# Performance work log

Measured on AMD Instinct MI355X. Metric: run time of the kernel, lower is better.

Reference implementation:

```python
import jax, jax.numpy as jnp
import numpy as np

B, HC, WC, KC = 4, 32, 32, 1024   # coarse feature map (ResNet101 layer3)
HF, WF, KF = 128, 128, 256        # fine feature map (ResNet101 layer1)
DC = 4                            # downscale_coef; HF // DC == HC


def setup_inputs() -> dict:
    key = jax.random.key(0)
    k1, k2, k3, k4 = jax.random.split(key, 4)
    return {
        "F_g1_coarse": jax.random.normal(k1, (B, HC, WC, KC), jnp.float32),
        "F_gk_coarse": jax.random.normal(k2, (B, HC, WC, KC), jnp.float32),
        "F_g1_fine": jax.random.normal(k3, (B, HF, WF, KF), jnp.float32),
        "F_gk_fine": jax.random.normal(k4, (B, HF, WF, KF), jnp.float32),
    }


def _coarse_match(f1, fk):
    # For every coarse position in Gk find nearest (L2) coarse position in G1.
    b, h, w, k = f1.shape
    a = f1.reshape(b, h * w, k)   # G1 positions
    q = fk.reshape(b, h * w, k)   # Gk positions
    # ||q||^2 + ||a||^2 - 2 q.a  -> [B, HW_gk, HW_g1]
    d = ((q * q).sum(-1)[:, :, None]
         + (a * a).sum(-1)[:, None, :]
         - 2.0 * jnp.einsum('bnk,bmk->bnm', q, a))
    idx = jnp.argmin(d, axis=-1)                       # [B, HW]
    cm = jnp.stack([idx // w, idx % w], axis=-1)       # (row, col) in G1
    return cm.reshape(b, h, w, 2).astype(jnp.int32)


def _fine_match(f1, fk, cm, dc):
    # Refine each dc x dc fine tile of Gk by searching the fine pixels of G1
    # covered by the coarse matches of the 3x3 coarse-neighborhood.
    b, h, w, k = fk.shape
    hc, wc = h // dc, w // dc
    off = jnp.arange(-1, 2)
    nI = jnp.clip(jnp.arange(hc)[:, None] + off[None, :], 0, hc - 1)  # [Hc,3]
    nJ = jnp.clip(jnp.arange(wc)[:, None] + off[None, :], 0, wc - 1)  # [Wc,3]
    # neighbor coarse matches: [B, Hc, Wc, 3, 3, 2]
    nb = cm[:, nI[:, None, :, None], nJ[None, :, None, :]]
    nb = nb.reshape(b, hc, wc, 9, 2)
    # expand each coarse match to its dc*dc fine pixels in G1
    sr = jnp.repeat(jnp.arange(dc), dc)   # [dc^2] row shifts
    sc = jnp.tile(jnp.arange(dc), dc)     # [dc^2] col shifts
    ncand = 9 * dc * dc                   # 144 candidates per tile
    cand_r = (nb[..., 0][..., None] * dc + sr).reshape(b, hc, wc, ncand)
    cand_c = (nb[..., 1][..., None] * dc + sc).reshape(b, hc, wc, ncand)
    # gather candidate fine features from G1: [B, Hc, Wc, N, K]
    bi = jnp.arange(b)[:, None, None, None]
    cand_f = f1[bi, cand_r, cand_c]
    # fine tile features of Gk: [B, Hc, Wc, dc^2, K]
    fkb = fk.reshape(b, hc, dc, wc, dc, k).transpose(0, 1, 3, 2, 4, 5)
    fkb = fkb.reshape(b, hc, wc, dc * dc, k)
    dist = ((fkb * fkb).sum(-1)[..., :, None]
            + (cand_f * cand_f).sum(-1)[..., None, :]
            - 2.0 * jnp.einsum('bhwpk,bhwnk->bhwpn', fkb, cand_f))
    best = jnp.argmin(dist, axis=-1)      # [B, Hc, Wc, dc^2]
    hi = jnp.arange(hc)[None, :, None, None]
    wi = jnp.arange(wc)[None, None, :, None]
    best_r = cand_r[bi, hi, wi, best]     # [B, Hc, Wc, dc^2]
    best_c = cand_c[bi, hi, wi, best]
    def to_grid(x):
        return x.reshape(b, hc, wc, dc, dc).transpose(0, 1, 3, 2, 4).reshape(b, h, w)
    return jnp.stack([to_grid(best_r), to_grid(best_c)], axis=-1).astype(jnp.int32)


def reference(F_g1_coarse, F_gk_coarse, F_g1_fine, F_gk_fine):
    closest_coarse = _coarse_match(F_g1_coarse, F_gk_coarse)   # [B,Hc,Wc,2]
    closest_fine = _fine_match(F_g1_fine, F_gk_fine, closest_coarse, DC)  # [B,H,W,2]
    return closest_coarse, closest_fine
```

## Files before the change

### kernel.cpp

```cpp
#include <hip/hip_runtime.h>
#include <cstdint>
#include <cstddef>

#define BB 4
#define HCC 32
#define WCC 32
#define KCC 1024
#define NCC (HCC*WCC)
#define HFF 128
#define WFF 128
#define KFF 256
#define DCC 4
#define NCHUNK 8

typedef _Float16 half8 __attribute__((ext_vector_type(8)));
typedef _Float16 half4_t __attribute__((ext_vector_type(4)));
typedef float f32x4 __attribute__((ext_vector_type(4)));
#define MFMA16(a,b,c) __builtin_amdgcn_mfma_f32_16x16x32_f16((a),(b),(c),0,0,0)
#define INV2K 0.00048828125f

__device__ inline void cvt8(const float4 u0, const float4 u1, half8& h, half8& l2) {
  float uu[8];
  *(float4*)uu = u0; *(float4*)(uu + 4) = u1;
  #pragma unroll
  for (int e = 0; e < 8; ++e) {
    _Float16 hh = (_Float16)uu[e];
    float r = (uu[e] - (float)hh) * 2048.0f;
    h[e] = hh; l2[e] = (_Float16)r;
  }
}

template<int K>
__global__ __launch_bounds__(256) void preconv_kernel(
    const float* __restrict__ src0, const float* __restrict__ src1,
    _Float16* __restrict__ hi0, _Float16* __restrict__ lo0,
    _Float16* __restrict__ hi1, _Float16* __restrict__ lo1,
    float* __restrict__ nr0, float* __restrict__ nr1, int rows) {
  const float* __restrict__ src = blockIdx.y ? src1 : src0;
  _Float16* __restrict__ hi = blockIdx.y ? hi1 : hi0;
  _Float16* __restrict__ lo = blockIdx.y ? lo1 : lo0;
  float* __restrict__ nrm = blockIdx.y ? nr1 : nr0;
  const int wave = threadIdx.x >> 6, lane = threadIdx.x & 63;
  const int row = blockIdx.x * 4 + wave;
  if (row >= rows) return;
  const float* p = src + (size_t)row * K;
  const size_t ob = (size_t)row * K + lane * 4;
  float s = 0.f;
  #pragma unroll
  for (int c = 0; c < K / 256; ++c) {
    float4 v = *(const float4*)(p + c * 256 + lane * 4);
    s += v.x*v.x + v.y*v.y + v.z*v.z + v.w*v.w;
    float vv[4] = {v.x, v.y, v.z, v.w};
    half4_t h, l2;
    #pragma unroll
    for (int e = 0; e < 4; ++e) {
      _Float16 hh = (_Float16)vv[e];
      l2[e] = (_Float16)((vv[e] - (float)hh) * 2048.0f);
      h[e] = hh;
    }
    *(half4_t*)(hi + ob + c * 256) = h;
    *(half4_t*)(lo + ob + c * 256) = l2;
  }
  #pragma unroll
  for (int m = 1; m <= 32; m <<= 1) s += __shfl_xor(s, m, 64);
  if (lane == 0) nrm[row] = s;
}

__global__ __launch_bounds__(256) void preconv_fine_kernel(
    const float* __restrict__ src, _Float16* __restrict__ hl,
    float* __restrict__ nrm, int rows) {
  const int wave = threadIdx.x >> 6, lane = threadIdx.x & 63;
  const int row = blockIdx.x * 4 + wave;
  if (row >= rows) return;
  float4 v = *(const float4*)(src + (size_t)row * KFF + lane * 4);
  float s = v.x*v.x + v.y*v.y + v.z*v.z + v.w*v.w;
  float vv[4] = {v.x, v.y, v.z, v.w};
  half4_t h, l2;
  #pragma unroll
  for (int e = 0; e < 4; ++e) {
    _Float16 hh = (_Float16)vv[e];
    l2[e] = (_Float16)((vv[e] - (float)hh) * 2048.0f);
    h[e] = hh;
  }
  const size_t dst = (size_t)row * 512 + (lane >> 3) * 64 + ((lane >> 1) & 3) * 16 + (lane & 1) * 4;
  *(half4_t*)(hl + dst)     = h;
  *(half4_t*)(hl + dst + 8) = l2;
  #pragma unroll
  for (int m = 1; m <= 32; m <<= 1) s += __shfl_xor(s, m, 64);
  if (lane == 0) nrm[row] = s;
}

__global__ __launch_bounds__(256, 2) void coarse_kernel2(
    const _Float16* __restrict__ gAhi, const _Float16* __restrict__ gAlo,
    const _Float16* __restrict__ gBhi, const _Float16* __restrict__ gBlo,
    const float* __restrict__ na, const float* __restrict__ nq,
    float* __restrict__ pval, int* __restrict__ pidx) {
  __shared__ _Float16 Ahi[128][64], Alo[128][64];
  __shared__ _Float16 Bhi[64][64],  Blo[64][64];
  __shared__ float a2s[128], q2s[64];
  __shared__ float redv[2][64];
  __shared__ int   redi[2][64];

  const int t = threadIdx.x;
  const int chunk = blockIdx.x;
  const int n0 = blockIdx.y * 64;
  const int b  = blockIdx.z;
  const int m0 = chunk * 128;

  const int ar = t >> 1, ahf = t & 1;
  const int brw = t >> 2, bq = t & 3;
  const int l  = t & 63;
  const int wv = t >> 6;
  const int wm = wv >> 1, wn = wv & 1;

  if (t < 128) a2s[t] = na[b*NCC + m0 + t];
  else if (t < 192) q2s[t - 128] = nq[b*NCC + n0 + (t - 128)];

  const _Float16* __restrict__ gah = gAhi + (size_t)(b*NCC + m0 + ar) * KCC + ahf * 32;
  const _Float16* __restrict__ gal = gAlo + (size_t)(b*NCC + m0 + ar) * KCC + ahf * 32;
  const _Float16* __restrict__ gbh = gBhi + (size_t)(b*NCC + n0 + brw) * KCC + bq * 16;
  const _Float16* __restrict__ gbl = gBlo + (size_t)(b*NCC + n0 + brw) * KCC + bq * 16;

  f32x4 accA[4][2], accB[4][2];
  #pragma unroll
  for (int mt = 0; mt < 4; ++mt)
    #pragma unroll
    for (int nt = 0; nt < 2; ++nt) { accA[mt][nt] = (f32x4)0.f; accB[mt][nt] = (f32x4)0.f; }

  for (int k0 = 0; k0 < KCC; k0 += 64) {
    __syncthreads();
    #pragma unroll
    for (int c2 = 0; c2 < 4; ++c2) {
      half8 h  = *(const half8*)(gah + k0 + c2 * 8);
      half8 l8 = *(const half8*)(gal + k0 + c2 * 8);
      int cs = (ahf * 4 + c2) ^ (ar & 7);
      *(half8*)&Ahi[ar][cs * 8] = h;
      *(half8*)&Alo[ar][cs * 8] = l8;
    }
    #pragma unroll
    for (int c2 = 0; c2 < 2; ++c2) {
      half8 h  = *(const half8*)(gbh + k0 + c2 * 8);
      half8 l8 = *(const half8*)(gbl + k0 + c2 * 8);
      int cs = (bq * 2 + c2) ^ (brw & 7);
      *(half8*)&Bhi[brw][cs * 8] = h;
      *(half8*)&Blo[brw][cs * 8] = l8;
    }
    __syncthreads();

    #pragma unroll
    for (int kk = 0; kk < 2; ++kk) {
      const int cs = ((kk * 4 + (l >> 4)) ^ (l & 7)) * 8;
      half8 ah[4], al[4], bh[2], bl[2];
      #pragma unroll
      for (int mt = 0; mt < 4; ++mt) {
        int row = wm * 64 + mt * 16 + (l & 15);
        ah[mt] = *(const half8*)&Ahi[row][cs];
        al[mt] = *(const half8*)&Alo[row][cs];
      }
      #pragma unroll
      for (int nt = 0; nt < 2; ++nt) {
        int row = wn * 32 + nt * 16 + (l & 15);
        bh[nt] = *(const half8*)&Bhi[row][cs];
        bl[nt] = *(const half8*)&Blo[row][cs];
      }
      #pragma unroll
      for (int mt = 0; mt < 4; ++mt)
        #pragma unroll
        for (int nt = 0; nt < 2; ++nt) {
          accA[mt][nt] = MFMA16(ah[mt], bh[nt], accA[mt][nt]);
          accB[mt][nt] = MFMA16(ah[mt], bl[nt], accB[mt][nt]);
          accB[mt][nt] = MFMA16(al[mt], bh[nt], accB[mt][nt]);
        }
    }
  }

  #pragma unroll
  for (int nt = 0; nt < 2; ++nt) {
    float q2 = q2s[wn * 32 + nt * 16 + (l & 15)];
    float bv = 3.0e38f; int bi = 0;
    #pragma unroll
    for (int mt = 0; mt < 4; ++mt)
      #pragma unroll
      for (int r = 0; r < 4; ++r) {
        float dot = accA[mt][nt][r] + accB[mt][nt][r] * INV2K;
        int ml = wm * 64 + mt * 16 + (l >> 4) * 4 + r;
        float d = (q2 + a2s[ml]) - 2.0f * dot;
        if (d < bv) { bv = d; bi = m0 + ml; }
      }
    #pragma unroll
    for (int mm = 16; mm < 64; mm <<= 1) {
      float ov = __shfl_xor(bv, mm, 64);
      int oi = __shfl_xor(bi, mm, 64);
      if (ov < bv || (ov == bv && oi < bi)) { bv = ov; bi = oi; }
    }
    if ((l >> 4) == 0) { redv[wm][wn*32 + nt*16 + l] = bv; redi[wm][wn*32 + nt*16 + l] = bi; }
  }
  __syncthreads();
  if (t < 64) {
    float v0 = redv[0][t]; int i0 = redi[0][t];
    float v1 = redv[1][t]; int i1 = redi[1][t];
    if (v1 < v0) { v0 = v1; i0 = i1; }
    pval[((size_t)b * NCC + n0 + t) * NCHUNK + chunk] = v0;
    pidx[((size_t)b * NCC + n0 + t) * NCHUNK + chunk] = i0;
  }
}

__global__ __launch_bounds__(256) void coarse_reduce_kernel(
    const float* __restrict__ pval, const int* __restrict__ pidx,
    int* __restrict__ out) {
  int g = blockIdx.x * 256 + threadIdx.x;
  if (g >= BB * NCC) return;
  float bv = pval[(size_t)g * NCHUNK];
  int bi = pidx[(size_t)g * NCHUNK];
  #pragma unroll
  for (int c = 1; c < NCHUNK; ++c) {
    float v = pval[(size_t)g * NCHUNK + c];
    int ix = pidx[(size_t)g * NCHUNK + c];
    if (v < bv) { bv = v; bi = ix; }
  }
  out[(size_t)g*2]     = bi >> 5;
  out[(size_t)g*2 + 1] = bi & 31;
}

__global__ __launch_bounds__(1024, 4) void fine_kernel4(
    const _Float16* __restrict__ gHL, const float* __restrict__ fkf,
    const float* __restrict__ naf, const int* __restrict__ coarse,
    int* __restrict__ outf) {
  __shared__ _Float16 CS[576 * 64];
  __shared__ _Float16 QS[256 * 64];
  __shared__ int   rIdx[576];
  __shared__ float tNORM[576];
  __shared__ float QN4[256][4];
  __shared__ int cbr[36], cbc[36];

  const int t = threadIdx.x;
  const int bx = blockIdx.x, by = blockIdx.y, b = blockIdx.z;
  const int l = t & 63, w = t >> 6;
  const int cy = w >> 2, cx = w & 3;
  const int ii = by * 4 + cy, jj = bx * 4 + cx;

  if (t < 36) {
    int wy = t / 6, wx = t % 6;
    int y = min(max(by * 4 - 1 + wy, 0), HCC - 1);
    int x = min(max(bx * 4 - 1 + wx, 0), WCC - 1);
    int base = ((b * HCC + y) * WCC + x) * 2;
    cbr[t] = coarse[base]; cbc[t] = coarse[base + 1];
  }
  __syncthreads();
  if (t < 576) {
    int slot = t >> 4, s = t & 15;
    int row = cbr[slot] * DCC + (s >> 2), col = cbc[slot] * DCC + (s & 3);
    int g = (b * HFF + row) * WFF + col;
    rIdx[t] = g; tNORM[t] = naf[g];
  }
  const int qrow = t >> 2, qpart = t & 3;
  const int qcell = qrow >> 4, qs = qrow & 15;
  const int qfr = (by * 4 + (qcell >> 2)) * DCC + (qs >> 2);
  const int qfc = (bx * 4 + (qcell & 3)) * DCC + (qs & 3);
  const float* qsrc = fkf + ((size_t)(b * HFF + qfr) * WFF + qfc) * KFF + qpart * 8;
  const int qswz = qrow & 7;
  float qnp = 0.f;
  __syncthreads();

  f32x4 accA[9], accB[9];
  #pragma unroll
  for (int T = 0; T < 9; ++T) { accA[T] = (f32x4)0.f; accB[T] = (f32x4)0.f; }

  const int q = l >> 4, r = l & 15;
  const int rsw = r & 7;
  const int woff[9] = {0, 1, 2, 6, 7, 8, 12, 13, 14};
  const int wbase = cy * 6 + cx;

  for (int ke = 0; ke < 8; ++ke) {
    #pragma unroll
    for (int it = 0; it < 5; ++it) {
      int g2 = it * 1024 + t;
      if (g2 < 4608) {
        int rowG = g2 >> 3, lc = g2 & 7;
        const _Float16* src = gHL + (size_t)rIdx[rowG] * 512 + ke * 64
                              + (lc >> 1) * 16 + (lc & 1) * 8;
        half8 v = *(const half8*)src;
        *(half8*)&CS[rowG * 64 + (lc ^ (rowG & 7)) * 8] = v;
      }
    }
    {
      float4 u0 = *(const float4*)(qsrc + ke * 32);
      float4 u1 = *(const float4*)(qsrc + ke * 32 + 4);
      qnp += u0.x*u0.x + u0.y*u0.y + u0.z*u0.z + u0.w*u0.w
           + u1.x*u1.x + u1.y*u1.y + u1.z*u1.z + u1.w*u1.w;
      half8 hh, hl;
      cvt8(u0, u1, hh, hl);
      *(half8*)&QS[qrow * 64 + ((qpart * 2)     ^ qswz) * 8] = hh;
      *(half8*)&QS[qrow * 64 + ((qpart * 2 + 1) ^ qswz) * 8] = hl;
      if (ke == 7) { QN4[qrow][qpart] = qnp; }
    }
    __syncthreads();
    half8 bh = *(const half8*)&QS[(w * 16 + r) * 64 + ((q * 2)     ^ rsw) * 8];
    half8 bl = *(const half8*)&QS[(w * 16 + r) * 64 + ((q * 2 + 1) ^ rsw) * 8];
    #pragma unroll
    for (int T = 0; T < 9; ++T) {
      int rowG = (wbase + woff[T]) * 16 + r;
      half8 ah = *(const half8*)&CS[rowG * 64 + ((q * 2)     ^ rsw) * 8];
      half8 al = *(const half8*)&CS[rowG * 64 + ((q * 2 + 1) ^ rsw) * 8];
      accA[T] = MFMA16(ah, bh, accA[T]);
      accB[T] = MFMA16(ah, bl, accB[T]);
      accB[T] = MFMA16(al, bh, accB[T]);
    }
    __syncthreads();
  }

  {
    float q2v = QN4[w * 16 + r][0] + QN4[w * 16 + r][1]
              + QN4[w * 16 + r][2] + QN4[w * 16 + r][3];
    float bv = 3.0e38f; int bi = 0;
    #pragma unroll
    for (int T = 0; T < 9; ++T) {
      int slot = wbase + woff[T];
      #pragma unroll
      for (int r2 = 0; r2 < 4; ++r2) {
        int s4 = q * 4 + r2;
        float cn = tNORM[slot * 16 + s4];
        float dot = accA[T][r2] + accB[T][r2] * INV2K;
        float d = (q2v + cn) - 2.0f * dot;
        int m = T * 16 + s4;
        if (d < bv) { bv = d; bi = m; }
      }
    }
    #pragma unroll
    for (int mm = 16; mm < 64; mm <<= 1) {
      float ov = __shfl_xor(bv, mm, 64);
      int oi = __shfl_xor(bi, mm, 64);
      if (ov < bv || (ov == bv && oi < bi)) { bv = ov; bi = oi; }
    }
    if (l < 16) {
      int T = bi >> 4, s3 = bi & 15, slot = wbase + woff[T];
      int br = cbr[slot] * DCC + (s3 >> 2);
      int bc = cbc[slot] * DCC + (s3 & 3);
      int fr = ii * DCC + (l >> 2), fc = jj * DCC + (l & 3);
      size_t ob = ((size_t)(b * HFF + fr) * WFF + fc) * 2;
      outf[ob]     = br;
      outf[ob + 1] = bc;
    }
  }
}

__global__ __launch_bounds__(256, 2) void coarse_kernel(
    const float* __restrict__ f1, const float* __restrict__ fk,
    float* __restrict__ pval, int* __restrict__ pidx) {
  __shared__ _Float16 Ahi[128][64], Alo[128][64];
  __shared__ _Float16 Bhi[64][64],  Blo[64][64];
  __shared__ float npA[256], npB[256];
  __shared__ float a2s[128], q2s[64];
  __shared__ float redv[2][64];
  __shared__ int   redi[2][64];

  const int t = threadIdx.x;
  const int chunk = blockIdx.x;
  const int n0 = blockIdx.y * 64;
  const int b  = blockIdx.z;
  const int m0 = chunk * 128;

  const float* __restrict__ Abase = f1 + ((size_t)b * NCC + m0) * KCC;
  const float* __restrict__ Bbase = fk + ((size_t)b * NCC + n0) * KCC;

  const int ar = t >> 1, ahf = t & 1;
  const int brw = t >> 2, bq = t & 3;
  const int l  = t & 63;
  const int wv = t >> 6;
  const int wm = wv >> 1, wn = wv & 1;

  float nrmA = 0.f, nrmB = 0.f;
  f32x4 accA[4][2], accB[4][2];
  #pragma unroll
  for (int mt = 0; mt < 4; ++mt)
    #pragma unroll
    for (int nt = 0; nt < 2; ++nt) { accA[mt][nt] = (f32x4)0.f; accB[mt][nt] = (f32x4)0.f; }

  for (int k0 = 0; k0 < KCC; k0 += 64) {
    __syncthreads();
    {
      const float4* src = (const float4*)(Abase + (size_t)ar * KCC + k0 + ahf * 32);
      float4 va[8];
      #pragma unroll
      for (int i2 = 0; i2 < 8; ++i2) va[i2] = src[i2];
      #pragma unroll
      for (int i2 = 0; i2 < 8; ++i2)
        nrmA += va[i2].x*va[i2].x + va[i2].y*va[i2].y + va[i2].z*va[i2].z + va[i2].w*va[i2].w;
      #pragma unroll
      for (int c2 = 0; c2 < 4; ++c2) {
        half8 hh, hl;
        cvt8(va[c2*2], va[c2*2+1], hh, hl);
        int cs = (ahf * 4 + c2) ^ (ar & 7);
        *(half8*)&Ahi[ar][cs * 8] = hh;
        *(half8*)&Alo[ar][cs * 8] = hl;
      }
    }
    {
      const float4* src = (const float4*)(Bbase + (size_t)brw * KCC + k0 + bq * 16);
      float4 vb[4];
      #pragma unroll
      for (int i2 = 0; i2 < 4; ++i2) vb[i2] = src[i2];
      #pragma unroll
      for (int i2 = 0; i2 < 4; ++i2)
        nrmB += vb[i2].x*vb[i2].x + vb[i2].y*vb[i2].y + vb[i2].z*vb[i2].z + vb[i2].w*vb[i2].w;
      #pragma unroll
      for (int c2 = 0; c2 < 2; ++c2) {
        half8 hh, hl;
        cvt8(vb[c2*2], vb[c2*2+1], hh, hl);
        int cs = (bq * 2 + c2) ^ (brw & 7);
        *(half8*)&Bhi[brw][cs * 8] = hh;
        *(half8*)&Blo[brw][cs * 8] = hl;
      }
    }
    __syncthreads();

    #pragma unroll
    for (int kk = 0; kk < 2; ++kk) {
      const int cs = ((kk * 4 + (l >> 4)) ^ (l & 7)) * 8;
      half8 ah[4], al[4], bh[2], bl[2];
      #pragma unroll
      for (int mt = 0; mt < 4; ++mt) {
        int row = wm * 64 + mt * 16 + (l & 15);
        ah[mt] = *(const half8*)&Ahi[row][cs];
        al[mt] = *(const half8*)&Alo[row][cs];
      }
      #pragma unroll
      for (int nt = 0; nt < 2; ++nt) {
        int row = wn * 32 + nt * 16 + (l & 15);
        bh[nt] = *(const half8*)&Bhi[row][cs];
        bl[nt] = *(const half8*)&Blo[row][cs];
      }
      #pragma unroll
      for (int mt = 0; mt < 4; ++mt)
        #pragma unroll
        for (int nt = 0; nt < 2; ++nt) {
          accA[mt][nt] = MFMA16(ah[mt], bh[nt], accA[mt][nt]);
          accB[mt][nt] = MFMA16(ah[mt], bl[nt], accB[mt][nt]);
          accB[mt][nt] = MFMA16(al[mt], bh[nt], accB[mt][nt]);
        }
    }
  }

  npA[t] = nrmA; npB[t] = nrmB;
  __syncthreads();
  if (t < 128) a2s[t] = npA[2*t] + npA[2*t + 1];
  if (t < 64)  q2s[t] = npB[4*t] + npB[4*t + 1] + npB[4*t + 2] + npB[4*t + 3];
  __syncthreads();

  #pragma unroll
  for (int nt = 0; nt < 2; ++nt) {
    float q2 = q2s[wn * 32 + nt * 16 + (l & 15)];
    float bv = 3.0e38f; int bi = 0;
    #pragma unroll
    for (int mt = 0; mt < 4; ++mt)
      #pragma unroll
      for (int r = 0; r < 4; ++r) {
        float dot = accA[mt][nt][r] + accB[mt][nt][r] * INV2K;
        int ml = wm * 64 + mt * 16 + (l >> 4) * 4 + r;
        float d = (q2 + a2s[ml]) - 2.0f * dot;
        if (d < bv) { bv = d; bi = m0 + ml; }
      }
    #pragma unroll
    for (int mm = 16; mm < 64; mm <<= 1) {
      float ov = __shfl_xor(bv, mm, 64);
      int oi = __shfl_xor(bi, mm, 64);
      if (ov < bv || (ov == bv && oi < bi)) { bv = ov; bi = oi; }
    }
    if ((l >> 4) == 0) { redv[wm][wn*32 + nt*16 + l] = bv; redi[wm][wn*32 + nt*16 + l] = bi; }
  }
  __syncthreads();
  if (t < 64) {
    float v0 = redv[0][t]; int i0 = redi[0][t];
    float v1 = redv[1][t]; int i1 = redi[1][t];
    if (v1 < v0) { v0 = v1; i0 = i1; }
    pval[((size_t)b * NCC + n0 + t) * NCHUNK + chunk] = v0;
    pidx[((size_t)b * NCC + n0 + t) * NCHUNK + chunk] = i0;
  }
}

__global__ __launch_bounds__(192) void fine_kernel(
    const float* __restrict__ f1, const float* __restrict__ fkf,
    const int* __restrict__ coarse, int* __restrict__ outf) {
  __shared__ _Float16 Qhi[16][256], Qlo[16][256];
  __shared__ float qn[16], cn[144];
  __shared__ int cROW[144];
  __shared__ int cbr[9], cbc[9];
  __shared__ float redv[3][16];
  __shared__ int   redi[3][16];

  const int t = threadIdx.x;
  const int j = blockIdx.x, i = blockIdx.y, b = blockIdx.z;
  const int l = t & 63, wv = t >> 6;

  if (t < 9) {
    int di = t / 3 - 1, dj = t % 3 - 1;
    int y = min(max(i + di, 0), HCC - 1);
    int x = min(max(j + dj, 0), WCC - 1);
    int base = ((b*HCC + y)*WCC + x) * 2;
    cbr[t] = coarse[base];
    cbc[t] = coarse[base + 1];
  }
  __syncthreads();
  if (t < 144) {
    int n9 = t >> 4, s = t & 15;
    int row = cbr[n9]*DCC + (s >> 2), col = cbc[n9]*DCC + (s & 3);
    cROW[t] = (b*HFF + row)*WFF + col;
  }
  if (t < 64) {
    int qr = l & 15, qq = l >> 4;
    int fr = i*DCC + (qr >> 2), fc = j*DCC + (qr & 3);
    const float* src = fkf + ((size_t)(b*HFF + fr)*WFF + fc) * KFF + qq * 64;
    float s2 = 0.f;
    #pragma unroll
    for (int c2 = 0; c2 < 8; ++c2) {
      float4 u0 = *(const float4*)(src + c2*8);
      float4 u1 = *(const float4*)(src + c2*8 + 4);
      s2 += u0.x*u0.x + u0.y*u0.y + u0.z*u0.z + u0.w*u0.w
          + u1.x*u1.x + u1.y*u1.y + u1.z*u1.z + u1.w*u1.w;
      half8 hh, hl;
      cvt8(u0, u1, hh, hl);
      int cs = (qq * 8 + c2) ^ (qr & 7);
      *(half8*)&Qhi[qr][cs * 8] = hh;
      *(half8*)&Qlo[qr][cs * 8] = hl;
    }
    s2 += __shfl_xor(s2, 16, 64);
    s2 += __shfl_xor(s2, 32, 64);
    if (qq == 0) qn[qr] = s2;
  }
  __syncthreads();

  const float* ap[3];
  #pragma unroll
  for (int T = 0; T < 3; ++T)
    ap[T] = f1 + (size_t)cROW[(wv*3 + T)*16 + (l & 15)] * KFF;

  f32x4 accA[3], accB[3];
  float nrmp[3];
  #pragma unroll
  for (int T = 0; T < 3; ++T) { accA[T] = (f32x4)0.f; accB[T] = (f32x4)0.f; nrmp[T] = 0.f; }

  #pragma unroll 2
  for (int s = 0; s < 8; ++s) {
    const int cs = ((s * 4 + (l >> 4)) ^ (l & 7)) * 8;
    half8 bh = *(const half8*)&Qhi[l & 15][cs];
    half8 bl = *(const half8*)&Qlo[l & 15][cs];
    #pragma unroll
    for (int T = 0; T < 3; ++T) {
      const float* p = ap[T] + s*32 + (l >> 4)*8;
      float4 u0 = *(const float4*)p;
      float4 u1 = *(const float4*)(p + 4);
      nrmp[T] += u0.x*u0.x + u0.y*u0.y + u0.z*u0.z + u0.w*u0.w
               + u1.x*u1.x + u1.y*u1.y + u1.z*u1.z + u1.w*u1.w;
      half8 ahv, alv;
      cvt8(u0, u1, ahv, alv);
      accA[T] = MFMA16(ahv, bh, accA[T]);
      accB[T] = MFMA16(ahv, bl, accB[T]);
      accB[T] = MFMA16(alv, bh, accB[T]);
    }
  }

  #pragma unroll
  for (int T = 0; T < 3; ++T) {
    float np = nrmp[T];
    np += __shfl_xor(np, 16, 64);
    np += __shfl_xor(np, 32, 64);
    if ((l >> 4) == 0) cn[(wv*3 + T)*16 + l] = np;
  }
  __syncthreads();

  {
    float q2 = qn[l & 15];
    float bv = 3.0e38f; int bi = 0;
    #pragma unroll
    for (int T = 0; T < 3; ++T)
      #pragma unroll
      for (int r = 0; r < 4; ++r) {
        float dot = accA[T][r] + accB[T][r] * INV2K;
        int m = (wv*3 + T)*16 + (l >> 4)*4 + r;
        float d = (q2 + cn[m]) - 2.0f * dot;
        if (d < bv) { bv = d; bi = m; }
      }
    #pragma unroll
    for (int mm = 16; mm < 64; mm <<= 1) {
      float ov = __shfl_xor(bv, mm, 64);
      int oi = __shfl_xor(bi, mm, 64);
      if (ov < bv || (ov == bv && oi < bi)) { bv = ov; bi = oi; }
    }
    if ((l >> 4) == 0 && l < 16) { redv[wv][l] = bv; redi[wv][l] = bi; }
  }
  __syncthreads();

  if (t < 16) {
    float v = redv[0][t]; int ix = redi[0][t];
    #pragma unroll
    for (int w = 1; w < 3; ++w) {
      float ov = redv[w][t];
      if (ov < v) { v = ov; ix = redi[w][t]; }
    }
    int n9 = ix >> 4, s3 = ix & 15;
    int br = cbr[n9]*DCC + (s3 >> 2);
    int bc = cbc[n9]*DCC + (s3 & 3);
    int fr = i*DCC + (t >> 2), fc = j*DCC + (t & 3);
    size_t ob = ((size_t)(b*HFF + fr)*WFF + fc) * 2;
    outf[ob]     = br;
    outf[ob + 1] = bc;
  }
}

extern "C" void kernel_launch(void* const* d_in, const int* in_sizes, int n_in,
                              void* d_out, int out_size, void* d_ws, size_t ws_size,
                              hipStream_t stream) {
  (void)in_sizes; (void)n_in; (void)out_size;
  const float* f1c = (const float*)d_in[0];
  const float* fkc = (const float*)d_in[1];
  const float* f1f = (const float*)d_in[2];
  const float* fkf = (const float*)d_in[3];
  int* out = (int*)d_out;

  const size_t NEED = 101220352;
  if (ws_size >= NEED) {
    char* w = (char*)d_ws;
    _Float16* cAhi = (_Float16*)(w);
    _Float16* cAlo = (_Float16*)(w + 8388608);
    _Float16* cBhi = (_Float16*)(w + 16777216);
    _Float16* cBlo = (_Float16*)(w + 25165824);
    _Float16* fHL  = (_Float16*)(w + 33554432);
    float* na_c = (float*)(w + 100663296);
    float* nq_c = (float*)(w + 100679680);
    float* na_f = (float*)(w + 100696064);
    float* pval = (float*)(w + 100958208);
    int*   pidx = (int*)  (w + 101089280);

    preconv_kernel<KCC><<<dim3(BB*NCC/4, 2), 256, 0, stream>>>(
        f1c, fkc, cAhi, cAlo, cBhi, cBlo, na_c, nq_c, BB*NCC);
    preconv_fine_kernel<<<dim3(BB*HFF*WFF/4), 256, 0, stream>>>(
        f1f, fHL, na_f, BB*HFF*WFF);
    coarse_kernel2<<<dim3(NCHUNK, NCC/64, BB), 256, 0, stream>>>(
        cAhi, cAlo, cBhi, cBlo, na_c, nq_c, pval, pidx);
    coarse_reduce_kernel<<<dim3((BB*NCC + 255)/256), 256, 0, stream>>>(pval, pidx, out);
    fine_kernel4<<<dim3(WCC/4, HCC/4, BB), 1024, 0, stream>>>(
        fHL, fkf, na_f, out, out + BB*NCC*2);
  } else {
    float* pval = (float*)d_ws;
    int*   pidx = (int*)((float*)d_ws + BB*NCC*NCHUNK);
    coarse_kernel<<<dim3(NCHUNK, NCC/64, BB), 256, 0, stream>>>(f1c, fkc, pval, pidx);
    coarse_reduce_kernel<<<dim3((BB*NCC + 255)/256), 256, 0, stream>>>(pval, pidx, out);
    fine_kernel<<<dim3(WCC, HCC, BB), 192, 0, stream>>>(f1f, fkf, out, out + BB*NCC*2);
  }
}
```

Measured before the change: 118.2 us.

## Register-prefetch next K tiles in coarse and fine kernels, shrink fine blocks

Both the coarse GEMM kernel and the fine matching kernel now load the next K-slice from global memory into registers while MFMAs run on the current shared-memory tile, hiding global load latency. The fine kernel is also reshaped from 1024-thread blocks covering 4x4 coarse cells to 512-thread blocks covering 2x4 cells. It precomputes gather offsets and drops the trailing barrier. This costs more registers and reloads more halo candidates per output, and the relaxed launch bounds may lower occupancy.

```diff
diff --git a/kernel.cpp b/kernel.cpp
--- a/kernel.cpp
+++ b/kernel.cpp
@@ -90,7 +90,7 @@
   if (lane == 0) nrm[row] = s;
 }
 
-__global__ __launch_bounds__(256, 2) void coarse_kernel2(
+__global__ __launch_bounds__(256) void coarse_kernel3(
     const _Float16* __restrict__ gAhi, const _Float16* __restrict__ gAlo,
     const _Float16* __restrict__ gBhi, const _Float16* __restrict__ gBlo,
     const float* __restrict__ na, const float* __restrict__ nq,
@@ -127,25 +127,40 @@
     #pragma unroll
     for (int nt = 0; nt < 2; ++nt) { accA[mt][nt] = (f32x4)0.f; accB[mt][nt] = (f32x4)0.f; }
 
+  half8 pah[4], pal[4], pbh[2], pbl[2];
+  #pragma unroll
+  for (int c2 = 0; c2 < 4; ++c2) { pah[c2] = *(const half8*)(gah + c2*8); pal[c2] = *(const half8*)(gal + c2*8); }
+  #pragma unroll
+  for (int c2 = 0; c2 < 2; ++c2) { pbh[c2] = *(const half8*)(gbh + c2*8); pbl[c2] = *(const half8*)(gbl + c2*8); }
+
   for (int k0 = 0; k0 < KCC; k0 += 64) {
     __syncthreads();
     #pragma unroll
     for (int c2 = 0; c2 < 4; ++c2) {
-      half8 h  = *(const half8*)(gah + k0 + c2 * 8);
-      half8 l8 = *(const half8*)(gal + k0 + c2 * 8);
       int cs = (ahf * 4 + c2) ^ (ar & 7);
-      *(half8*)&Ahi[ar][cs * 8] = h;
-      *(half8*)&Alo[ar][cs * 8] = l8;
+      *(half8*)&Ahi[ar][cs * 8] = pah[c2];
+      *(half8*)&Alo[ar][cs * 8] = pal[c2];
     }
     #pragma unroll
     for (int c2 = 0; c2 < 2; ++c2) {
-      half8 h  = *(const half8*)(gbh + k0 + c2 * 8);
-      half8 l8 = *(const half8*)(gbl + k0 + c2 * 8);
       int cs = (bq * 2 + c2) ^ (brw & 7);
-      *(half8*)&Bhi[brw][cs * 8] = h;
-      *(half8*)&Blo[brw][cs * 8] = l8;
+      *(half8*)&Bhi[brw][cs * 8] = pbh[c2];
+      *(half8*)&Blo[brw][cs * 8] = pbl[c2];
     }
     __syncthreads();
+
+    if (k0 + 64 < KCC) {
+      #pragma unroll
+      for (int c2 = 0; c2 < 4; ++c2) {
+        pah[c2] = *(const half8*)(gah + k0 + 64 + c2*8);
+        pal[c2] = *(const half8*)(gal + k0 + 64 + c2*8);
+      }
+      #pragma unroll
+      for (int c2 = 0; c2 < 2; ++c2) {
+        pbh[c2] = *(const half8*)(gbh + k0 + 64 + c2*8);
+        pbl[c2] = *(const half8*)(gbl + k0 + 64 + c2*8);
+      }
+    }
 
     #pragma unroll
     for (int kk = 0; kk < 2; ++kk) {
@@ -222,45 +237,60 @@
   out[(size_t)g*2 + 1] = bi & 31;
 }
 
-__global__ __launch_bounds__(1024, 4) void fine_kernel4(
+__global__ __launch_bounds__(512) void fine_kernel5(
     const _Float16* __restrict__ gHL, const float* __restrict__ fkf,
     const float* __restrict__ naf, const int* __restrict__ coarse,
     int* __restrict__ outf) {
-  __shared__ _Float16 CS[576 * 64];
-  __shared__ _Float16 QS[256 * 64];
-  __shared__ int   rIdx[576];
-  __shared__ float tNORM[576];
-  __shared__ float QN4[256][4];
-  __shared__ int cbr[36], cbc[36];
+  __shared__ _Float16 CS[384 * 64];
+  __shared__ _Float16 QS[128 * 64];
+  __shared__ int   rIdx[384];
+  __shared__ float tNORM[384];
+  __shared__ float QN4[128][4];
+  __shared__ int cbr[24], cbc[24];
 
   const int t = threadIdx.x;
   const int bx = blockIdx.x, by = blockIdx.y, b = blockIdx.z;
   const int l = t & 63, w = t >> 6;
   const int cy = w >> 2, cx = w & 3;
-  const int ii = by * 4 + cy, jj = bx * 4 + cx;
-
-  if (t < 36) {
+  const int ii = by * 2 + cy, jj = bx * 4 + cx;
+
+  if (t < 24) {
     int wy = t / 6, wx = t % 6;
-    int y = min(max(by * 4 - 1 + wy, 0), HCC - 1);
+    int y = min(max(by * 2 - 1 + wy, 0), HCC - 1);
     int x = min(max(bx * 4 - 1 + wx, 0), WCC - 1);
     int base = ((b * HCC + y) * WCC + x) * 2;
     cbr[t] = coarse[base]; cbc[t] = coarse[base + 1];
   }
   __syncthreads();
-  if (t < 576) {
+  if (t < 384) {
     int slot = t >> 4, s = t & 15;
     int row = cbr[slot] * DCC + (s >> 2), col = cbc[slot] * DCC + (s & 3);
     int g = (b * HFF + row) * WFF + col;
     rIdx[t] = g; tNORM[t] = naf[g];
   }
+  __syncthreads();
+
+  unsigned srcOff[6], dstOff[6];
+  #pragma unroll
+  for (int it = 0; it < 6; ++it) {
+    int g2 = it * 512 + t;
+    int rowG = g2 >> 3, lc = g2 & 7;
+    srcOff[it] = (unsigned)rIdx[rowG] * 512u + (unsigned)((lc >> 1) * 16 + (lc & 1) * 8);
+    dstOff[it] = (unsigned)(rowG * 64 + (lc ^ (rowG & 7)) * 8);
+  }
   const int qrow = t >> 2, qpart = t & 3;
   const int qcell = qrow >> 4, qs = qrow & 15;
-  const int qfr = (by * 4 + (qcell >> 2)) * DCC + (qs >> 2);
+  const int qfr = (by * 2 + (qcell >> 2)) * DCC + (qs >> 2);
   const int qfc = (bx * 4 + (qcell & 3)) * DCC + (qs & 3);
   const float* qsrc = fkf + ((size_t)(b * HFF + qfr) * WFF + qfc) * KFF + qpart * 8;
   const int qswz = qrow & 7;
   float qnp = 0.f;
-  __syncthreads();
+
+  half8 pf[6];
+  #pragma unroll
+  for (int it = 0; it < 6; ++it) pf[it] = *(const half8*)(gHL + srcOff[it]);
+  float4 qu0 = *(const float4*)(qsrc);
+  float4 qu1 = *(const float4*)(qsrc + 4);
 
   f32x4 accA[9], accB[9];
   #pragma unroll
@@ -272,29 +302,28 @@
   const int wbase = cy * 6 + cx;
 
   for (int ke = 0; ke < 8; ++ke) {
-    #pragma unroll
-    for (int it = 0; it < 5; ++it) {
-      int g2 = it * 1024 + t;
-      if (g2 < 4608) {
-        int rowG = g2 >> 3, lc = g2 & 7;
-        const _Float16* src = gHL + (size_t)rIdx[rowG] * 512 + ke * 64
-                              + (lc >> 1) * 16 + (lc & 1) * 8;
-        half8 v = *(const half8*)src;
-        *(half8*)&CS[rowG * 64 + (lc ^ (rowG & 7)) * 8] = v;
-      }
-    }
+    __syncthreads();
+    #pragma unroll
+    for (int it = 0; it < 6; ++it) *(half8*)&CS[dstOff[it]] = pf[it];
     {
-      float4 u0 = *(const float4*)(qsrc + ke * 32);
-      float4 u1 = *(const float4*)(qsrc + ke * 32 + 4);
-      qnp += u0.x*u0.x + u0.y*u0.y + u0.z*u0.z + u0.w*u0.w
-           + u1.x*u1.x + u1.y*u1.y + u1.z*u1.z + u1.w*u1.w;
+      qnp += qu0.x*qu0.x + qu0.y*qu0.y + qu0.z*qu0.z + qu0.w*qu0.w
+           + qu1.x*qu1.x + qu1.y*qu1.y + qu1.z*qu1.z + qu1.w*qu1.w;
       half8 hh, hl;
-      cvt8(u0, u1, hh, hl);
+      cvt8(qu0, qu1, hh, hl);
       *(half8*)&QS[qrow * 64 + ((qpart * 2)     ^ qswz) * 8] = hh;
       *(half8*)&QS[qrow * 64 + ((qpart * 2 + 1) ^ qswz) * 8] = hl;
-      if (ke == 7) { QN4[qrow][qpart] = qnp; }
+      if (ke == 7) QN4[qrow][qpart] = qnp;
     }
     __syncthreads();
+
+    if (ke < 7) {
+      #pragma unroll
+      for (int it = 0; it < 6; ++it)
+        pf[it] = *(const half8*)(gHL + srcOff[it] + (unsigned)(ke + 1) * 64u);
+      qu0 = *(const float4*)(qsrc + (ke + 1) * 32);
+      qu1 = *(const float4*)(qsrc + (ke + 1) * 32 + 4);
+    }
+
     half8 bh = *(const half8*)&QS[(w * 16 + r) * 64 + ((q * 2)     ^ rsw) * 8];
     half8 bl = *(const half8*)&QS[(w * 16 + r) * 64 + ((q * 2 + 1) ^ rsw) * 8];
     #pragma unroll
@@ -306,7 +335,6 @@
       accB[T] = MFMA16(ah, bl, accB[T]);
       accB[T] = MFMA16(al, bh, accB[T]);
     }
-    __syncthreads();
   }
 
   {
@@ -635,10 +663,10 @@
         f1c, fkc, cAhi, cAlo, cBhi, cBlo, na_c, nq_c, BB*NCC);
     preconv_fine_kernel<<<dim3(BB*HFF*WFF/4), 256, 0, stream>>>(
         f1f, fHL, na_f, BB*HFF*WFF);
-    coarse_kernel2<<<dim3(NCHUNK, NCC/64, BB), 256, 0, stream>>>(
+    coarse_kernel3<<<dim3(NCHUNK, NCC/64, BB), 256, 0, stream>>>(
         cAhi, cAlo, cBhi, cBlo, na_c, nq_c, pval, pidx);
     coarse_reduce_kernel<<<dim3((BB*NCC + 255)/256), 256, 0, stream>>>(pval, pidx, out);
-    fine_kernel4<<<dim3(WCC/4, HCC/4, BB), 1024, 0, stream>>>(
+    fine_kernel5<<<dim3(WCC/4, HCC/2, BB), 512, 0, stream>>>(
         fHL, fkf, na_f, out, out + BB*NCC*2);
   } else {
     float* pval = (float*)d_ws;
```

Measured after the change: 112.4 us. 4.9% less time.
